# Performance work log

Measured on AMD Instinct MI355X. Metric: run time of the kernel, lower is better.

## Reference

```python
import jax, jax.numpy as jnp
import numpy as np
import math

M = 0.5
S = 30.0
COS_M = math.cos(M)
SIN_M = math.sin(M)


def setup_inputs() -> dict:
    key = jax.random.key(0)
    k1, k2, k3 = jax.random.split(key, 3)
    batch, din, nclass = 512, 512, 100000
    x = jax.random.normal(k1, (batch, din), dtype=jnp.float32)
    # xavier_uniform for weight (out, in)
    limit = math.sqrt(6.0 / (nclass + din))
    w = jax.random.uniform(k2, (nclass, din), dtype=jnp.float32, minval=-limit, maxval=limit)
    target = jax.random.randint(k3, (batch,), 0, nclass, dtype=jnp.int64)
    return {"input": x, "weight": w, "target": target}


def reference(input, weight, target):
    # L2-normalize rows (torch F.normalize uses eps=1e-12 clamp on norm)
    xn = input / jnp.maximum(jnp.linalg.norm(input, axis=1, keepdims=True), 1e-12)
    wn = weight / jnp.maximum(jnp.linalg.norm(weight, axis=1, keepdims=True), 1e-12)
    cosine = xn @ wn.T  # [B, C]
    sine = jnp.sqrt(jnp.maximum(1.0 - cosine * cosine, 0.0))
    phi = cosine * COS_M - sine * SIN_M
    # easy_margin=True
    phi = jnp.where(cosine > 0, phi, cosine)
    one_hot = jax.nn.one_hot(target, cosine.shape[1], dtype=cosine.dtype)  # [B, C]
    logits = S * (one_hot * phi + (1.0 - one_hot) * cosine)
    # cross-entropy with mean reduction
    logp = jax.nn.log_softmax(logits, axis=1)
    nll = -jnp.take_along_axis(logp, target[:, None], axis=1)[:, 0]
    return jnp.mean(nll)
```

## Files before the change

### kernel.cpp

```cpp
#include <hip/hip_runtime.h>
#include <math.h>

#define BATCH 512
#define DIM 512
#define NCLASS 100000
#define BN 64
#define NBLK ((NCLASS + BN - 1) / BN)
#define S_SCALE 30.0f
#define COSM 0.8775825618903728f
#define SINM 0.4794255386042030f

typedef unsigned short u16;
typedef __attribute__((ext_vector_type(8))) short short8;
typedef __attribute__((ext_vector_type(4))) float floatx4;


__device__ __forceinline__ u16 f2bf(float f) {
    union { float f; unsigned int u; } v;
    v.f = f;
    unsigned int u = v.u;
    u += 0x7fffu + ((u >> 16) & 1u);
    return (u16)(u >> 16);
}

__global__ void xnorm_kernel(const float* __restrict__ x, u16* __restrict__ xn) {
    const int row = blockIdx.x;
    const int t = threadIdx.x;
    const floatx4* xr = (const floatx4*)(x + (size_t)row * DIM);
    floatx4 a = xr[t];
    floatx4 b = xr[t + 64];
    float ss = a[0]*a[0] + a[1]*a[1] + a[2]*a[2] + a[3]*a[3]
             + b[0]*b[0] + b[1]*b[1] + b[2]*b[2] + b[3]*b[3];
#pragma unroll
    for (int d = 1; d < 64; d <<= 1) ss += __shfl_xor(ss, d);
    const float rn = 1.0f / fmaxf(sqrtf(ss), 1e-12f);
    ushort4 ua, ub;
    ua.x = f2bf(a[0]*rn); ua.y = f2bf(a[1]*rn); ua.z = f2bf(a[2]*rn); ua.w = f2bf(a[3]*rn);
    ub.x = f2bf(b[0]*rn); ub.y = f2bf(b[1]*rn); ub.z = f2bf(b[2]*rn); ub.w = f2bf(b[3]*rn);
    u16* orow = xn + (size_t)row * DIM;
    *(ushort4*)(orow + 4*t)       = ua;
    *(ushort4*)(orow + 256 + 4*t) = ub;
}

__global__ void arcface_main(const float* __restrict__ w,
                             const u16* __restrict__ xn,
                             const int* __restrict__ target,
                             float* __restrict__ partials,
                             float* __restrict__ tlogit) {
    __shared__ u16 wb[BN * DIM];

    const int c0 = blockIdx.x * BN;
    const int t = threadIdx.x;

    {
        const int r = t >> 3;
        const int q = t & 7;
        const int cg = c0 + r;
        floatx4 v[16];
        float ss = 0.f;
        if (cg < NCLASS) {
            const floatx4* wr = (const floatx4*)(w + (size_t)cg * DIM);
#pragma unroll
            for (int i = 0; i < 16; ++i) {
                v[i] = wr[q + (i << 3)];
                ss += v[i][0]*v[i][0] + v[i][1]*v[i][1] + v[i][2]*v[i][2] + v[i][3]*v[i][3];
            }
        } else {
#pragma unroll
            for (int i = 0; i < 16; ++i) { v[i][0]=0.f; v[i][1]=0.f; v[i][2]=0.f; v[i][3]=0.f; }
        }
        ss += __shfl_xor(ss, 1);
        ss += __shfl_xor(ss, 2);
        ss += __shfl_xor(ss, 4);
        const float rs = 1.0f / fmaxf(sqrtf(ss), 1e-12f);
#pragma unroll
        for (int i = 0; i < 16; ++i) {
            const int col4 = q + (i << 3);
            const int gp = (col4 >> 1) ^ (r & 7);
            const int off = r * DIM + gp * 8 + (col4 & 1) * 4;
            ushort4 u;
            u.x = f2bf(v[i][0] * rs); u.y = f2bf(v[i][1] * rs);
            u.z = f2bf(v[i][2] * rs); u.w = f2bf(v[i][3] * rs);
            *(ushort4*)(&wb[off]) = u;
        }
    }
    __syncthreads();

    const int wave = t >> 6;
    const int lane = t & 63;
    const int quad = lane >> 4;
    const int nin  = lane & 15;
    const int mbase = wave * 64;

    floatx4 acc[4][4];
#pragma unroll
    for (int mi = 0; mi < 4; ++mi)
#pragma unroll
        for (int ni = 0; ni < 4; ++ni) {
            acc[mi][ni][0] = 0.f; acc[mi][ni][1] = 0.f;
            acc[mi][ni][2] = 0.f; acc[mi][ni][3] = 0.f;
        }

    for (int kk = 0; kk < 16; ++kk) {
        short8 a[4], b[4];
        const int k = kk * 32 + quad * 8;
#pragma unroll
        for (int mi = 0; mi < 4; ++mi) {
            const int m = mbase + mi * 16 + nin;
            a[mi] = *(const short8*)(xn + (size_t)m * DIM + k);
        }
#pragma unroll
        for (int ni = 0; ni < 4; ++ni) {
            const int cl = ni * 16 + nin;
            const int gp = ((kk << 2) + quad) ^ (cl & 7);
            b[ni] = *(const short8*)(&wb[cl * DIM + gp * 8]);
        }
#pragma unroll
        for (int mi = 0; mi < 4; ++mi)
#pragma unroll
            for (int ni = 0; ni < 4; ++ni)
                acc[mi][ni] = __builtin_amdgcn_mfma_f32_16x16x32_bf16(
                    a[mi], b[ni], acc[mi][ni], 0, 0, 0);
    }

#pragma unroll
    for (int mi = 0; mi < 4; ++mi) {
#pragma unroll
        for (int reg = 0; reg < 4; ++reg) {
            const int m = mbase + mi * 16 + quad * 4 + reg;
            const int tg = target[m];
            float psum = 0.f;
#pragma unroll
            for (int ni = 0; ni < 4; ++ni) {
                const int c = c0 + ni * 16 + nin;
                if (c < NCLASS) {
                    const float cosv = acc[mi][ni][reg];
                    float lg;
                    if (c == tg) {
                        const float sine = sqrtf(fmaxf(1.f - cosv * cosv, 0.f));
                        float phi = cosv * COSM - sine * SINM;
                        if (!(cosv > 0.f)) phi = cosv;
                        lg = S_SCALE * phi;
                        tlogit[m] = lg;
                    } else {
                        lg = S_SCALE * cosv;
                    }
                    psum += __expf(lg - S_SCALE);
                }
            }
            psum += __shfl_xor(psum, 1);
            psum += __shfl_xor(psum, 2);
            psum += __shfl_xor(psum, 4);
            psum += __shfl_xor(psum, 8);
            if (nin == 0)
                partials[(size_t)blockIdx.x * BATCH + m] = psum;
        }
    }
}

__global__ void reduce_lse(const float* __restrict__ partials,
                           const float* __restrict__ tlogit,
                           float* __restrict__ nll) {
    const int m = blockIdx.x;
    const int t = threadIdx.x;
    float s = 0.f;
    for (int b = t; b < NBLK; b += 256) s += partials[(size_t)b * BATCH + m];
#pragma unroll
    for (int d = 1; d < 64; d <<= 1) s += __shfl_xor(s, d);
    __shared__ float red[4];
    if ((t & 63) == 0) red[t >> 6] = s;
    __syncthreads();
    if (t == 0) {
        const float tot = red[0] + red[1] + red[2] + red[3];
        nll[m] = (logf(tot) + S_SCALE) - tlogit[m];
    }
}

__global__ void reduce_mean(const float* __restrict__ nll, float* __restrict__ out) {
    const int t = threadIdx.x;
    float s = nll[t];
#pragma unroll
    for (int d = 1; d < 64; d <<= 1) s += __shfl_xor(s, d);
    __shared__ float red[8];
    if ((t & 63) == 0) red[t >> 6] = s;
    __syncthreads();
    if (t == 0) {
        float tot = 0.f;
#pragma unroll
        for (int i = 0; i < 8; ++i) tot += red[i];
        out[0] = tot / (float)BATCH;
    }
}

extern "C" void kernel_launch(void* const* d_in, const int* in_sizes, int n_in,
                              void* d_out, int out_size, void* d_ws, size_t ws_size,
                              hipStream_t stream) {
    const float* x = (const float*)d_in[0];
    const float* w = (const float*)d_in[1];
    const int* target = (const int*)d_in[2];

    char* ws = (char*)d_ws;
    u16* xn        = (u16*)ws;
    float* tlogit  = (float*)(ws + 524288);
    float* nll     = (float*)(ws + 526336);
    float* partials= (float*)(ws + 528384);

    xnorm_kernel<<<BATCH, 64, 0, stream>>>(x, xn);
    arcface_main<<<NBLK, 512, 0, stream>>>(w, xn, target, partials, tlogit);
    reduce_lse<<<BATCH, 256, 0, stream>>>(partials, tlogit, nll);
    reduce_mean<<<1, 512, 0, stream>>>(nll, (float*)d_out);
}
```

Before: 404.2 us.

## Make arcface main kernel persistent with register-prefetched weight tiles

Replaces the one-block-per-tile launch with 256 persistent blocks that loop over class tiles. The global loads for the next tile's weights are issued into registers before the current tile's MFMA work and committed to shared memory afterwards. The k loop is double-buffered for the A and B fragments, targets are hoisted into registers, and the partials layout is transposed to row-major so the reduction reads contiguously. Using 256 blocks with launch_bounds(512,2) may underfill the GPU. The 64 extra prefetch registers per thread add register pressure.

```diff
diff --git a/kernel.cpp b/kernel.cpp
--- a/kernel.cpp
+++ b/kernel.cpp
@@ -5,7 +5,8 @@
 #define DIM 512
 #define NCLASS 100000
 #define BN 64
-#define NBLK ((NCLASS + BN - 1) / BN)
+#define NT 1563
+#define NBLOCKS 256
 #define S_SCALE 30.0f
 #define COSM 0.8775825618903728f
 #define SINM 0.4794255386042030f
@@ -42,49 +43,54 @@
     *(ushort4*)(orow + 256 + 4*t) = ub;
 }
 
-__global__ void arcface_main(const float* __restrict__ w,
-                             const u16* __restrict__ xn,
-                             const int* __restrict__ target,
-                             float* __restrict__ partials,
-                             float* __restrict__ tlogit) {
+__device__ __forceinline__ void stage_issue(const float* __restrict__ w, int cg, int sq,
+                                            floatx4* v) {
+    if (cg < NCLASS) {
+        const floatx4* wr = (const floatx4*)(w + (size_t)cg * DIM);
+#pragma unroll
+        for (int j = 0; j < 16; ++j) v[j] = wr[sq + (j << 3)];
+    } else {
+#pragma unroll
+        for (int j = 0; j < 16; ++j) { v[j][0]=0.f; v[j][1]=0.f; v[j][2]=0.f; v[j][3]=0.f; }
+    }
+}
+
+__device__ __forceinline__ void stage_commit(const floatx4* v, int sr, int sq,
+                                             u16* wb) {
+    float ss = 0.f;
+#pragma unroll
+    for (int j = 0; j < 16; ++j)
+        ss += v[j][0]*v[j][0] + v[j][1]*v[j][1] + v[j][2]*v[j][2] + v[j][3]*v[j][3];
+    ss += __shfl_xor(ss, 1);
+    ss += __shfl_xor(ss, 2);
+    ss += __shfl_xor(ss, 4);
+    const float rs = 1.0f / fmaxf(sqrtf(ss), 1e-12f);
+#pragma unroll
+    for (int j = 0; j < 16; ++j) {
+        const int col4 = sq + (j << 3);
+        const int gp = (col4 >> 1) ^ (sr & 7);
+        const int off = sr * DIM + gp * 8 + (col4 & 1) * 4;
+        ushort4 u;
+        u.x = f2bf(v[j][0] * rs); u.y = f2bf(v[j][1] * rs);
+        u.z = f2bf(v[j][2] * rs); u.w = f2bf(v[j][3] * rs);
+        *(ushort4*)(&wb[off]) = u;
+    }
+}
+
+__global__ __launch_bounds__(512, 2)
+void arcface_main(const float* __restrict__ w,
+                  const u16* __restrict__ xn,
+                  const int* __restrict__ target,
+                  float* __restrict__ partials,
+                  float* __restrict__ tlogit) {
     __shared__ u16 wb[BN * DIM];
 
-    const int c0 = blockIdx.x * BN;
-    const int t = threadIdx.x;
-
-    {
-        const int r = t >> 3;
-        const int q = t & 7;
-        const int cg = c0 + r;
-        floatx4 v[16];
-        float ss = 0.f;
-        if (cg < NCLASS) {
-            const floatx4* wr = (const floatx4*)(w + (size_t)cg * DIM);
-#pragma unroll
-            for (int i = 0; i < 16; ++i) {
-                v[i] = wr[q + (i << 3)];
-                ss += v[i][0]*v[i][0] + v[i][1]*v[i][1] + v[i][2]*v[i][2] + v[i][3]*v[i][3];
-            }
-        } else {
-#pragma unroll
-            for (int i = 0; i < 16; ++i) { v[i][0]=0.f; v[i][1]=0.f; v[i][2]=0.f; v[i][3]=0.f; }
-        }
-        ss += __shfl_xor(ss, 1);
-        ss += __shfl_xor(ss, 2);
-        ss += __shfl_xor(ss, 4);
-        const float rs = 1.0f / fmaxf(sqrtf(ss), 1e-12f);
-#pragma unroll
-        for (int i = 0; i < 16; ++i) {
-            const int col4 = q + (i << 3);
-            const int gp = (col4 >> 1) ^ (r & 7);
-            const int off = r * DIM + gp * 8 + (col4 & 1) * 4;
-            ushort4 u;
-            u.x = f2bf(v[i][0] * rs); u.y = f2bf(v[i][1] * rs);
-            u.z = f2bf(v[i][2] * rs); u.w = f2bf(v[i][3] * rs);
-            *(ushort4*)(&wb[off]) = u;
-        }
-    }
-    __syncthreads();
+    const int t = threadIdx.x;
+    const int bid = blockIdx.x;
+    const int cnt = (bid < (NT % NBLOCKS)) ? (NT / NBLOCKS + 1) : (NT / NBLOCKS);
+
+    const int sr = t >> 3;
+    const int sq = t & 7;
 
     const int wave = t >> 6;
     const int lane = t & 63;
@@ -92,69 +98,121 @@
     const int nin  = lane & 15;
     const int mbase = wave * 64;
 
-    floatx4 acc[4][4];
+    int tgv[4][4];
 #pragma unroll
     for (int mi = 0; mi < 4; ++mi)
 #pragma unroll
-        for (int ni = 0; ni < 4; ++ni) {
-            acc[mi][ni][0] = 0.f; acc[mi][ni][1] = 0.f;
-            acc[mi][ni][2] = 0.f; acc[mi][ni][3] = 0.f;
-        }
-
-    for (int kk = 0; kk < 16; ++kk) {
-        short8 a[4], b[4];
-        const int k = kk * 32 + quad * 8;
-#pragma unroll
-        for (int mi = 0; mi < 4; ++mi) {
-            const int m = mbase + mi * 16 + nin;
-            a[mi] = *(const short8*)(xn + (size_t)m * DIM + k);
-        }
+        for (int reg = 0; reg < 4; ++reg)
+            tgv[mi][reg] = target[mbase + mi * 16 + quad * 4 + reg];
+
+    floatx4 v[16];
+
+    stage_issue(w, bid * BN + sr, sq, v);
+    stage_commit(v, sr, sq, wb);
+    __syncthreads();
+
+    for (int i = 0; i < cnt; ++i) {
+        const int tile = bid + i * NBLOCKS;
+        const int c0 = tile * BN;
+        const bool hasNext = (i + 1 < cnt);
+
+        if (hasNext)
+            stage_issue(w, (bid + (i + 1) * NBLOCKS) * BN + sr, sq, v);
+
+        floatx4 acc[4][4];
+#pragma unroll
+        for (int mi = 0; mi < 4; ++mi)
+#pragma unroll
+            for (int ni = 0; ni < 4; ++ni) {
+                acc[mi][ni][0] = 0.f; acc[mi][ni][1] = 0.f;
+                acc[mi][ni][2] = 0.f; acc[mi][ni][3] = 0.f;
+            }
+
+        short8 a0[4], b0[4], a1[4], b1[4];
+#pragma unroll
+        for (int mi = 0; mi < 4; ++mi)
+            a0[mi] = *(const short8*)(xn + ((size_t)(mbase + mi * 16 + nin) << 9) + (quad << 3));
 #pragma unroll
         for (int ni = 0; ni < 4; ++ni) {
             const int cl = ni * 16 + nin;
-            const int gp = ((kk << 2) + quad) ^ (cl & 7);
-            b[ni] = *(const short8*)(&wb[cl * DIM + gp * 8]);
+            const int gp = quad ^ (cl & 7);
+            b0[ni] = *(const short8*)(&wb[(cl << 9) + (gp << 3)]);
         }
-#pragma unroll
-        for (int mi = 0; mi < 4; ++mi)
-#pragma unroll
-            for (int ni = 0; ni < 4; ++ni)
-                acc[mi][ni] = __builtin_amdgcn_mfma_f32_16x16x32_bf16(
-                    a[mi], b[ni], acc[mi][ni], 0, 0, 0);
-    }
-
-#pragma unroll
-    for (int mi = 0; mi < 4; ++mi) {
-#pragma unroll
-        for (int reg = 0; reg < 4; ++reg) {
-            const int m = mbase + mi * 16 + quad * 4 + reg;
-            const int tg = target[m];
-            float psum = 0.f;
+
+#pragma unroll
+        for (int kk = 0; kk < 16; kk += 2) {
+#pragma unroll
+            for (int mi = 0; mi < 4; ++mi)
+                a1[mi] = *(const short8*)(xn + ((size_t)(mbase + mi * 16 + nin) << 9)
+                                              + ((kk + 1) << 5) + (quad << 3));
 #pragma unroll
             for (int ni = 0; ni < 4; ++ni) {
-                const int c = c0 + ni * 16 + nin;
-                if (c < NCLASS) {
-                    const float cosv = acc[mi][ni][reg];
-                    float lg;
-                    if (c == tg) {
-                        const float sine = sqrtf(fmaxf(1.f - cosv * cosv, 0.f));
-                        float phi = cosv * COSM - sine * SINM;
-                        if (!(cosv > 0.f)) phi = cosv;
-                        lg = S_SCALE * phi;
-                        tlogit[m] = lg;
-                    } else {
-                        lg = S_SCALE * cosv;
+                const int cl = ni * 16 + nin;
+                const int gp = (((kk + 1) << 2) + quad) ^ (cl & 7);
+                b1[ni] = *(const short8*)(&wb[(cl << 9) + (gp << 3)]);
+            }
+#pragma unroll
+            for (int mi = 0; mi < 4; ++mi)
+#pragma unroll
+                for (int ni = 0; ni < 4; ++ni)
+                    acc[mi][ni] = __builtin_amdgcn_mfma_f32_16x16x32_bf16(
+                        a0[mi], b0[ni], acc[mi][ni], 0, 0, 0);
+            if (kk + 2 < 16) {
+#pragma unroll
+                for (int mi = 0; mi < 4; ++mi)
+                    a0[mi] = *(const short8*)(xn + ((size_t)(mbase + mi * 16 + nin) << 9)
+                                                  + ((kk + 2) << 5) + (quad << 3));
+#pragma unroll
+                for (int ni = 0; ni < 4; ++ni) {
+                    const int cl = ni * 16 + nin;
+                    const int gp = (((kk + 2) << 2) + quad) ^ (cl & 7);
+                    b0[ni] = *(const short8*)(&wb[(cl << 9) + (gp << 3)]);
+                }
+            }
+#pragma unroll
+            for (int mi = 0; mi < 4; ++mi)
+#pragma unroll
+                for (int ni = 0; ni < 4; ++ni)
+                    acc[mi][ni] = __builtin_amdgcn_mfma_f32_16x16x32_bf16(
+                        a1[mi], b1[ni], acc[mi][ni], 0, 0, 0);
+        }
+
+#pragma unroll
+        for (int mi = 0; mi < 4; ++mi) {
+#pragma unroll
+            for (int reg = 0; reg < 4; ++reg) {
+                const int m = mbase + mi * 16 + quad * 4 + reg;
+                const int tg = tgv[mi][reg];
+                float psum = 0.f;
+#pragma unroll
+                for (int ni = 0; ni < 4; ++ni) {
+                    const int c = c0 + ni * 16 + nin;
+                    if (c < NCLASS) {
+                        const float cosv = acc[mi][ni][reg];
+                        float lg = S_SCALE * cosv;
+                        if (c == tg) {
+                            const float sine = sqrtf(fmaxf(1.f - cosv * cosv, 0.f));
+                            float phi = cosv * COSM - sine * SINM;
+                            if (!(cosv > 0.f)) phi = cosv;
+                            lg = S_SCALE * phi;
+                            tlogit[m] = lg;
+                        }
+                        psum += __expf(lg - S_SCALE);
                     }
-                    psum += __expf(lg - S_SCALE);
                 }
-            }
-            psum += __shfl_xor(psum, 1);
-            psum += __shfl_xor(psum, 2);
-            psum += __shfl_xor(psum, 4);
-            psum += __shfl_xor(psum, 8);
-            if (nin == 0)
-                partials[(size_t)blockIdx.x * BATCH + m] = psum;
+                psum += __shfl_xor(psum, 1);
+                psum += __shfl_xor(psum, 2);
+                psum += __shfl_xor(psum, 4);
+                psum += __shfl_xor(psum, 8);
+                if (nin == 0)
+                    partials[(size_t)m * NT + tile] = psum;
+            }
         }
+
+        __syncthreads();
+        if (hasNext)
+            stage_commit(v, sr, sq, wb);
+        __syncthreads();
     }
 }
 
@@ -163,8 +221,9 @@
                            float* __restrict__ nll) {
     const int m = blockIdx.x;
     const int t = threadIdx.x;
+    const float* row = partials + (size_t)m * NT;
     float s = 0.f;
-    for (int b = t; b < NBLK; b += 256) s += partials[(size_t)b * BATCH + m];
+    for (int j = t; j < NT; j += 256) s += row[j];
 #pragma unroll
     for (int d = 1; d < 64; d <<= 1) s += __shfl_xor(s, d);
     __shared__ float red[4];
@@ -200,13 +259,13 @@
     const int* target = (const int*)d_in[2];
 
     char* ws = (char*)d_ws;
-    u16* xn        = (u16*)ws;
-    float* tlogit  = (float*)(ws + 524288);
-    float* nll     = (float*)(ws + 526336);
-    float* partials= (float*)(ws + 528384);
+    u16* xn         = (u16*)ws;
+    float* tlogit   = (float*)(ws + 524288);
+    float* nll      = (float*)(ws + 526336);
+    float* partials = (float*)(ws + 528384);
 
     xnorm_kernel<<<BATCH, 64, 0, stream>>>(x, xn);
-    arcface_main<<<NBLK, 512, 0, stream>>>(w, xn, target, partials, tlogit);
+    arcface_main<<<NBLOCKS, 512, 0, stream>>>(w, xn, target, partials, tlogit);
     reduce_lse<<<BATCH, 256, 0, stream>>>(partials, tlogit, nll);
     reduce_mean<<<1, 512, 0, stream>>>(nll, (float*)d_out);
 }
```

Result: slower. 583.2 us (+44.3%).

## Pipeline weight tiles via async global-to-LDS copies and defer normalization to epilogue

Applied to the files above, without the earlier changes.

The main kernel no longer loads the whole 64x512 fp32 weight tile into registers up front and normalizes it before any MFMA work. It now streams the tile in K-chunks of 64 with double-buffered global_load_lds async copies, converting each chunk to bf16 while the next chunk loads. Row sums of squares are accumulated in shared memory, and the inverse norm is applied to the accumulated dot products in the epilogue. This is meant to overlap the weight reads with compute and to cut register pressure and LDS footprint so more blocks can be resident. In exchange it adds two barriers per K-step and rounds unnormalized weights to bf16, which slightly changes numerics.

```diff
diff --git a/kernel.cpp b/kernel.cpp
--- a/kernel.cpp
+++ b/kernel.cpp
@@ -1,11 +1,14 @@
 #include <hip/hip_runtime.h>
 #include <math.h>
+#include <stdint.h>
 
 #define BATCH 512
 #define DIM 512
 #define NCLASS 100000
 #define BN 64
-#define NBLK ((NCLASS + BN - 1) / BN)
+#define BK 64
+#define NSTEP (DIM / BK)
+#define NT ((NCLASS + BN - 1) / BN)
 #define S_SCALE 30.0f
 #define COSM 0.8775825618903728f
 #define SINM 0.4794255386042030f
@@ -21,6 +24,14 @@
     unsigned int u = v.u;
     u += 0x7fffu + ((u >> 16) & 1u);
     return (u16)(u >> 16);
+}
+
+__device__ __forceinline__ void async_cp16(const void* g, void* l) {
+    auto gp = reinterpret_cast<const __attribute__((address_space(1))) unsigned int*>(
+        reinterpret_cast<uintptr_t>(g));
+    auto lp = reinterpret_cast<__attribute__((address_space(3))) unsigned int*>(
+        reinterpret_cast<uintptr_t>(l));
+    __builtin_amdgcn_global_load_lds(gp, lp, 16, 0, 0);
 }
 
 __global__ void xnorm_kernel(const float* __restrict__ x, u16* __restrict__ xn) {
@@ -47,44 +58,13 @@
                              const int* __restrict__ target,
                              float* __restrict__ partials,
                              float* __restrict__ tlogit) {
-    __shared__ u16 wb[BN * DIM];
-
-    const int c0 = blockIdx.x * BN;
-    const int t = threadIdx.x;
-
-    {
-        const int r = t >> 3;
-        const int q = t & 7;
-        const int cg = c0 + r;
-        floatx4 v[16];
-        float ss = 0.f;
-        if (cg < NCLASS) {
-            const floatx4* wr = (const floatx4*)(w + (size_t)cg * DIM);
-#pragma unroll
-            for (int i = 0; i < 16; ++i) {
-                v[i] = wr[q + (i << 3)];
-                ss += v[i][0]*v[i][0] + v[i][1]*v[i][1] + v[i][2]*v[i][2] + v[i][3]*v[i][3];
-            }
-        } else {
-#pragma unroll
-            for (int i = 0; i < 16; ++i) { v[i][0]=0.f; v[i][1]=0.f; v[i][2]=0.f; v[i][3]=0.f; }
-        }
-        ss += __shfl_xor(ss, 1);
-        ss += __shfl_xor(ss, 2);
-        ss += __shfl_xor(ss, 4);
-        const float rs = 1.0f / fmaxf(sqrtf(ss), 1e-12f);
-#pragma unroll
-        for (int i = 0; i < 16; ++i) {
-            const int col4 = q + (i << 3);
-            const int gp = (col4 >> 1) ^ (r & 7);
-            const int off = r * DIM + gp * 8 + (col4 & 1) * 4;
-            ushort4 u;
-            u.x = f2bf(v[i][0] * rs); u.y = f2bf(v[i][1] * rs);
-            u.z = f2bf(v[i][2] * rs); u.w = f2bf(v[i][3] * rs);
-            *(ushort4*)(&wb[off]) = u;
-        }
-    }
-    __syncthreads();
+    __shared__ float fbuf[2][BN * BK];
+    __shared__ u16   bbuf[BN * BK];
+    __shared__ float ssb[BN];
+
+    const int t = threadIdx.x;
+    const int tile = blockIdx.x;
+    const int c0 = tile * BN;
 
     const int wave = t >> 6;
     const int lane = t & 63;
@@ -92,6 +72,24 @@
     const int nin  = lane & 15;
     const int mbase = wave * 64;
 
+    size_t goff[2];
+    int ldsoff[2];
+#pragma unroll
+    for (int j = 0; j < 2; ++j) {
+        const int gi = wave * 128 + j * 64 + lane;
+        const int cl = gi >> 4, gq = gi & 15;
+        int cls = c0 + cl; if (cls > NCLASS - 1) cls = NCLASS - 1;
+        goff[j] = (size_t)cls * (DIM * 4) + (size_t)gq * 16;
+        ldsoff[j] = wave * 2048 + j * 1024;
+    }
+    const char* wbytes = (const char*)w;
+
+#pragma unroll
+    for (int j = 0; j < 2; ++j)
+        async_cp16(wbytes + goff[j], (char*)&fbuf[0][0] + ldsoff[j]);
+
+    if (t < BN) ssb[t] = 0.f;
+
     floatx4 acc[4][4];
 #pragma unroll
     for (int mi = 0; mi < 4; ++mi)
@@ -101,27 +99,66 @@
             acc[mi][ni][2] = 0.f; acc[mi][ni][3] = 0.f;
         }
 
-    for (int kk = 0; kk < 16; ++kk) {
-        short8 a[4], b[4];
-        const int k = kk * 32 + quad * 8;
-#pragma unroll
-        for (int mi = 0; mi < 4; ++mi) {
-            const int m = mbase + mi * 16 + nin;
-            a[mi] = *(const short8*)(xn + (size_t)m * DIM + k);
-        }
-#pragma unroll
-        for (int ni = 0; ni < 4; ++ni) {
-            const int cl = ni * 16 + nin;
-            const int gp = ((kk << 2) + quad) ^ (cl & 7);
-            b[ni] = *(const short8*)(&wb[cl * DIM + gp * 8]);
-        }
-#pragma unroll
-        for (int mi = 0; mi < 4; ++mi)
-#pragma unroll
-            for (int ni = 0; ni < 4; ++ni)
-                acc[mi][ni] = __builtin_amdgcn_mfma_f32_16x16x32_bf16(
-                    a[mi], b[ni], acc[mi][ni], 0, 0, 0);
-    }
+    const int scl  = t >> 3;
+    const int ssub = t & 7;
+
+    for (int ks = 0; ks < NSTEP; ++ks) {
+        const int p = ks & 1;
+        __syncthreads();
+
+        {
+            const floatx4 f0 = *(const floatx4*)((const char*)&fbuf[p][0] + t * 32);
+            const floatx4 f1 = *(const floatx4*)((const char*)&fbuf[p][0] + t * 32 + 16);
+            float ss = f0[0]*f0[0] + f0[1]*f0[1] + f0[2]*f0[2] + f0[3]*f0[3]
+                     + f1[0]*f1[0] + f1[1]*f1[1] + f1[2]*f1[2] + f1[3]*f1[3];
+            ss += __shfl_xor(ss, 1);
+            ss += __shfl_xor(ss, 2);
+            ss += __shfl_xor(ss, 4);
+            short8 br;
+            br[0] = (short)f2bf(f0[0]); br[1] = (short)f2bf(f0[1]);
+            br[2] = (short)f2bf(f0[2]); br[3] = (short)f2bf(f0[3]);
+            br[4] = (short)f2bf(f1[0]); br[5] = (short)f2bf(f1[1]);
+            br[6] = (short)f2bf(f1[2]); br[7] = (short)f2bf(f1[3]);
+            const int gsw = ssub ^ (scl & 7);
+            *(short8*)(&bbuf[scl * BK + gsw * 8]) = br;
+            if (ssub == 0) ssb[scl] += ss;
+        }
+        __syncthreads();
+
+        if (ks + 1 < NSTEP) {
+            const size_t so = (size_t)(ks + 1) * (BK * 4);
+#pragma unroll
+            for (int j = 0; j < 2; ++j)
+                async_cp16(wbytes + goff[j] + so, (char*)&fbuf[p ^ 1][0] + ldsoff[j]);
+        }
+
+#pragma unroll
+        for (int kk = 0; kk < 2; ++kk) {
+            short8 a[4], b[4];
+            const int kg = ks * BK + kk * 32 + quad * 8;
+#pragma unroll
+            for (int mi = 0; mi < 4; ++mi)
+                a[mi] = *(const short8*)(xn + (size_t)(mbase + mi * 16 + nin) * DIM + kg);
+#pragma unroll
+            for (int ni = 0; ni < 4; ++ni) {
+                const int cl = ni * 16 + nin;
+                const int g = kk * 4 + quad;
+                const int gsw = g ^ (cl & 7);
+                b[ni] = *(const short8*)(&bbuf[cl * BK + gsw * 8]);
+            }
+#pragma unroll
+            for (int mi = 0; mi < 4; ++mi)
+#pragma unroll
+                for (int ni = 0; ni < 4; ++ni)
+                    acc[mi][ni] = __builtin_amdgcn_mfma_f32_16x16x32_bf16(
+                        a[mi], b[ni], acc[mi][ni], 0, 0, 0);
+        }
+    }
+
+    float rns[4];
+#pragma unroll
+    for (int ni = 0; ni < 4; ++ni)
+        rns[ni] = 1.0f / fmaxf(sqrtf(ssb[ni * 16 + nin]), 1e-12f);
 
 #pragma unroll
     for (int mi = 0; mi < 4; ++mi) {
@@ -134,16 +171,14 @@
             for (int ni = 0; ni < 4; ++ni) {
                 const int c = c0 + ni * 16 + nin;
                 if (c < NCLASS) {
-                    const float cosv = acc[mi][ni][reg];
-                    float lg;
+                    const float cosv = acc[mi][ni][reg] * rns[ni];
+                    float lg = S_SCALE * cosv;
                     if (c == tg) {
                         const float sine = sqrtf(fmaxf(1.f - cosv * cosv, 0.f));
                         float phi = cosv * COSM - sine * SINM;
                         if (!(cosv > 0.f)) phi = cosv;
                         lg = S_SCALE * phi;
                         tlogit[m] = lg;
-                    } else {
-                        lg = S_SCALE * cosv;
                     }
                     psum += __expf(lg - S_SCALE);
                 }
@@ -153,7 +188,7 @@
             psum += __shfl_xor(psum, 4);
             psum += __shfl_xor(psum, 8);
             if (nin == 0)
-                partials[(size_t)blockIdx.x * BATCH + m] = psum;
+                partials[(size_t)tile * BATCH + m] = psum;
         }
     }
 }
@@ -164,7 +199,7 @@
     const int m = blockIdx.x;
     const int t = threadIdx.x;
     float s = 0.f;
-    for (int b = t; b < NBLK; b += 256) s += partials[(size_t)b * BATCH + m];
+    for (int b = t; b < NT; b += 256) s += partials[(size_t)b * BATCH + m];
 #pragma unroll
     for (int d = 1; d < 64; d <<= 1) s += __shfl_xor(s, d);
     __shared__ float red[4];
@@ -200,13 +235,13 @@
     const int* target = (const int*)d_in[2];
 
     char* ws = (char*)d_ws;
-    u16* xn        = (u16*)ws;
-    float* tlogit  = (float*)(ws + 524288);
-    float* nll     = (float*)(ws + 526336);
-    float* partials= (float*)(ws + 528384);
+    u16* xn         = (u16*)ws;
+    float* tlogit   = (float*)(ws + 524288);
+    float* nll      = (float*)(ws + 526336);
+    float* partials = (float*)(ws + 528384);
 
     xnorm_kernel<<<BATCH, 64, 0, stream>>>(x, xn);
-    arcface_main<<<NBLK, 512, 0, stream>>>(w, xn, target, partials, tlogit);
+    arcface_main<<<NT, 512, 0, stream>>>(w, xn, target, partials, tlogit);
     reduce_lse<<<BATCH, 256, 0, stream>>>(partials, tlogit, nll);
     reduce_mean<<<1, 512, 0, stream>>>(nll, (float*)d_out);
 }
```

Result: slower. 423.9 us (+4.9%).
